# Kernel optimization log

Hardware: AMD Instinct MI355X
Metric: run time of the kernel (lower is better)

The kernel has to match this reference:

```python
import jax, jax.numpy as jnp
import numpy as np

N_CENTER, N_NEAR, N_STEPK, N_HOPS = 512, 32, 10, 2
FEAT_NAMES = ["xyz_fea", "pmt_fea", "mad_fea", "dim_fea", "nor_fea", "loc_fea", "fea"]


def pairwise_sqdist(x):
    # x: [B,N,C] -> [B,N,N]
    xx = jnp.sum(x * x, axis=-1)
    return xx[:, :, None] + xx[:, None, :] - 2.0 * jnp.einsum('bnc,bmc->bnm', x, x)


def surface_knn(x, n_near, n_stepk, n_hops=N_HOPS):
    # Iterative surface-KNN: build a step-KNN graph with n_stepk neighbors,
    # expand the neighborhood n_hops times (neighbor-of-neighbor union), then
    # pick the n_near nearest points among the reachable candidate set.
    d = pairwise_sqdist(x)                      # [B,N,N]
    B, N, _ = d.shape
    _, nbr = jax.lax.top_k(-d, n_stepk + 1)     # step neighbors (incl. self)
    b_idx = jnp.arange(B)[:, None, None]
    r_idx = jnp.arange(N)[None, :, None]
    adj = jnp.zeros((B, N, N), jnp.bool_).at[b_idx, r_idx, nbr].set(True)
    reach = adj
    adj_f = adj.astype(jnp.float32)
    for _ in range(n_hops):
        reach = (jnp.einsum('bij,bjk->bik', reach.astype(jnp.float32), adj_f) > 0) | adj
    dm = jnp.where(reach, d, jnp.inf)
    _, idx = jax.lax.top_k(-dm, n_near)         # [B,N,n_near], nearest reachable
    return idx


def fps(x, n_center):
    # Farthest point sampling in the C-dim feature space (dim=dim in source).
    B, N, _ = x.shape
    d = pairwise_sqdist(x)
    barange = jnp.arange(B)

    def step(carry, _):
        mind, prev = carry
        mind = jnp.minimum(mind, d[barange, prev])   # [B,N]
        nxt = jnp.argmax(mind, axis=-1).astype(jnp.int32)
        return (mind, nxt), nxt

    init = (jnp.full((B, N), jnp.inf, jnp.float32), jnp.zeros((B,), jnp.int32))
    _, rest = jax.lax.scan(step, init, None, length=n_center - 1)  # [S-1,B]
    idx = jnp.concatenate([jnp.zeros((1, B), jnp.int32), rest], axis=0)
    return idx.T                                   # [B,S]


def branch(center, grouped, wq, bq, wk, bk, wv, bv, w1, b1, w2, b2):
    # center: [B,S,C], grouped: [B,S,K,C]
    C = center.shape[-1]
    q = center @ wq + bq                           # [B,S,C]
    k = grouped @ wk + bk                          # [B,S,K,C]
    v = grouped @ wv + bv
    scores = jnp.einsum('bsc,bskc->bsk', q, k) / jnp.sqrt(jnp.float32(C))
    attn = jax.nn.softmax(scores, axis=-1)
    out = jnp.einsum('bsk,bskc->bsc', attn, v)     # attention pooling -> [B,S,C]
    h = jax.nn.relu(out @ w1 + b1)                 # MLP (C -> Cout -> Cout)
    return jax.nn.relu(h @ w2 + b2)


def setup_inputs() -> dict:
    key = jax.random.key(0)
    ks = jax.random.split(key, 16)
    B, N, C, CO = 8, 2048, 128, 256
    inp = {}
    for i, name in enumerate(FEAT_NAMES):
        inp[name] = jax.random.normal(ks[i], (B, N, C), jnp.float32)
    s = np.float32(1.0 / np.sqrt(C))
    so = np.float32(1.0 / np.sqrt(CO))
    inp['aw_q'] = jax.random.normal(ks[7], (7, C, C), jnp.float32) * s
    inp['ab_q'] = jnp.zeros((7, C), jnp.float32)
    inp['aw_k'] = jax.random.normal(ks[8], (7, C, C), jnp.float32) * s
    inp['ab_k'] = jnp.zeros((7, C), jnp.float32)
    inp['aw_v'] = jax.random.normal(ks[9], (7, C, C), jnp.float32) * s
    inp['ab_v'] = jnp.zeros((7, C), jnp.float32)
    inp['mw1'] = jax.random.normal(ks[10], (7, C, CO), jnp.float32) * s
    inp['mb1'] = jnp.zeros((7, CO), jnp.float32)
    inp['mw2'] = jax.random.normal(ks[11], (7, CO, CO), jnp.float32) * so
    inp['mb2'] = jnp.zeros((7, CO), jnp.float32)
    return inp


def reference(xyz_fea, pmt_fea, mad_fea, dim_fea, nor_fea, loc_fea, fea,
              aw_q, ab_q, aw_k, ab_k, aw_v, ab_v, mw1, mb1, mw2, mb2):
    B = xyz_fea.shape[0]
    feats = jnp.stack([xyz_fea, pmt_fea, mad_fea, dim_fea, nor_fea, loc_fea, fea], 0)  # [7,B,N,C]
    idx_all = surface_knn(xyz_fea, N_NEAR, N_STEPK)      # [B,N,K]
    fps_idx = fps(xyz_fea, N_CENTER)                     # [B,S]
    b2 = jnp.arange(B)[:, None]                          # [B,1]
    b3 = jnp.arange(B)[:, None, None]                    # [B,1,1]
    centers = feats[:, b2, fps_idx]                      # [7,B,S,C]
    idx = idx_all[b2, fps_idx]                           # [B,S,K]
    grouped = feats[:, b3, idx]                          # [7,B,S,K,C]
    outs = jax.vmap(branch)(centers, grouped, aw_q, ab_q, aw_k, ab_k,
                            aw_v, ab_v, mw1, mb1, mw2, mb2)  # [7,B,S,CO]
    return tuple(outs[i] for i in range(7))
```

## Files before the change

### kernel.cpp

```cpp
#include <hip/hip_runtime.h>
#include <hip/hip_bf16.h>
#include <math.h>

constexpr int BATCH = 8;
constexpr int NPTS  = 2048;
constexpr int CH    = 128;
constexpr int CHO   = 256;
constexpr int NCEN  = 512;
constexpr int NNEI  = 32;
constexpr int NTOP  = 11;
constexpr int NW    = 64;
constexpr int SMEM_BYTES = 17408;
constexpr int SMEM_MID   = 20608;

struct Ptr7 { const float* p[7]; };

__global__ __launch_bounds__(256) void xx_kernel(const float* __restrict__ x,
                                                 float* __restrict__ xx) {
    int p = blockIdx.x * 256 + threadIdx.x;
    if (p >= BATCH * NPTS) return;
    const float4* xr = (const float4*)(x + (size_t)p * CH);
    float s = 0.f;
#pragma unroll
    for (int i = 0; i < CH / 4; i++) {
        float4 v = xr[i];
        s += v.x * v.x + v.y * v.y + v.z * v.z + v.w * v.w;
    }
    xx[p] = s;
}

__global__ __launch_bounds__(256) void dmat_kernel(const float* __restrict__ x,
                                                   const float* __restrict__ xx,
                                                   float* __restrict__ D) {
    __shared__ __align__(16) char smem[SMEM_BYTES];
    int it = blockIdx.y, jt = blockIdx.x;
    if (jt < it) return;
    float (*As)[68] = (float(*)[68])smem;
    float (*Bs)[68] = (float(*)[68])(smem + 32 * 68 * 4);
    int bz = blockIdx.z;
    int i0 = it * 64, j0 = jt * 64;
    const float* X = x + (size_t)bz * NPTS * CH;
    int t = threadIdx.x, tx = t & 15, ty = t >> 4;
    int lr = t >> 3, lc = (t & 7) * 4;
    const float* ai0 = X + (size_t)(i0 + lr) * CH;
    const float* ai1 = X + (size_t)(i0 + lr + 32) * CH;
    const float* bj0 = X + (size_t)(j0 + lr) * CH;
    const float* bj1 = X + (size_t)(j0 + lr + 32) * CH;
    float acc[4][4] = {};
    for (int kc = 0; kc < CH; kc += 32) {
        float4 a0 = *(const float4*)(ai0 + kc + lc);
        float4 a1 = *(const float4*)(ai1 + kc + lc);
        float4 b0 = *(const float4*)(bj0 + kc + lc);
        float4 b1 = *(const float4*)(bj1 + kc + lc);
        __syncthreads();
        As[lc + 0][lr] = a0.x; As[lc + 1][lr] = a0.y; As[lc + 2][lr] = a0.z; As[lc + 3][lr] = a0.w;
        As[lc + 0][lr + 32] = a1.x; As[lc + 1][lr + 32] = a1.y; As[lc + 2][lr + 32] = a1.z; As[lc + 3][lr + 32] = a1.w;
        Bs[lc + 0][lr] = b0.x; Bs[lc + 1][lr] = b0.y; Bs[lc + 2][lr] = b0.z; Bs[lc + 3][lr] = b0.w;
        Bs[lc + 0][lr + 32] = b1.x; Bs[lc + 1][lr + 32] = b1.y; Bs[lc + 2][lr + 32] = b1.z; Bs[lc + 3][lr + 32] = b1.w;
        __syncthreads();
#pragma unroll
        for (int kk = 0; kk < 32; kk++) {
            float4 av = *(const float4*)&As[kk][ty * 4];
            float4 bv = *(const float4*)&Bs[kk][tx * 4];
            float a[4] = {av.x, av.y, av.z, av.w};
            float b[4] = {bv.x, bv.y, bv.z, bv.w};
#pragma unroll
            for (int i = 0; i < 4; i++)
#pragma unroll
                for (int j = 0; j < 4; j++) acc[i][j] += a[i] * b[j];
        }
    }
    const float* xxb = xx + bz * NPTS;
    float xi[4], xj[4];
#pragma unroll
    for (int i = 0; i < 4; i++) xi[i] = xxb[i0 + ty * 4 + i];
#pragma unroll
    for (int j = 0; j < 4; j++) xj[j] = xxb[j0 + tx * 4 + j];
    float ov[4][4];
#pragma unroll
    for (int i = 0; i < 4; i++)
#pragma unroll
        for (int j = 0; j < 4; j++) ov[i][j] = xi[i] + xj[j] - 2.f * acc[i][j];
#pragma unroll
    for (int i = 0; i < 4; i++) {
        float4 o = {ov[i][0], ov[i][1], ov[i][2], ov[i][3]};
        *(float4*)(D + ((size_t)bz * NPTS + i0 + ty * 4 + i) * NPTS + j0 + tx * 4) = o;
    }
    if (jt > it) {
        __syncthreads();
        float (*T)[65] = (float(*)[65])smem;
#pragma unroll
        for (int i = 0; i < 4; i++)
#pragma unroll
            for (int j = 0; j < 4; j++) T[ty * 4 + i][tx * 4 + j] = ov[i][j];
        __syncthreads();
#pragma unroll
        for (int i = 0; i < 4; i++) {
            float4 o;
            o.x = T[tx * 4 + 0][ty * 4 + i];
            o.y = T[tx * 4 + 1][ty * 4 + i];
            o.z = T[tx * 4 + 2][ty * 4 + i];
            o.w = T[tx * 4 + 3][ty * 4 + i];
            *(float4*)(D + ((size_t)bz * NPTS + j0 + ty * 4 + i) * NPTS + i0 + tx * 4) = o;
        }
    }
}

__global__ __launch_bounds__(256) void fused_front_kernel(const float* __restrict__ D,
                                                          unsigned int* __restrict__ adj,
                                                          int* __restrict__ fps_idx) {
    __shared__ __align__(16) char smem[SMEM_BYTES];
    if (blockIdx.x < BATCH) {
        int lane = threadIdx.x;
        if (lane >= 64) return;
        int b = blockIdx.x;
        float mind[32];
#pragma unroll
        for (int r = 0; r < 32; r++) mind[r] = INFINITY;
        int prev = 0;
        if (lane == 0) fps_idx[b * NCEN] = 0;
        const float* Db = D + (size_t)b * NPTS * NPTS;
        for (int s = 1; s < NCEN; s++) {
            const float4* rowp = (const float4*)(Db + (size_t)prev * NPTS);
            float4 v0 = rowp[lane + 0 * 64];
            float4 v1 = rowp[lane + 1 * 64];
            float4 v2 = rowp[lane + 2 * 64];
            float4 v3 = rowp[lane + 3 * 64];
            float4 v4 = rowp[lane + 4 * 64];
            float4 v5 = rowp[lane + 5 * 64];
            float4 v6 = rowp[lane + 6 * 64];
            float4 v7 = rowp[lane + 7 * 64];
            float bv = -INFINITY; int bj = NPTS;
            float4 vv[8] = {v0, v1, v2, v3, v4, v5, v6, v7};
#pragma unroll
            for (int k = 0; k < 8; k++) {
                int j0 = 4 * (lane + 64 * k);
                float m0 = fminf(mind[4 * k + 0], vv[k].x); mind[4 * k + 0] = m0;
                float m1 = fminf(mind[4 * k + 1], vv[k].y); mind[4 * k + 1] = m1;
                float m2 = fminf(mind[4 * k + 2], vv[k].z); mind[4 * k + 2] = m2;
                float m3 = fminf(mind[4 * k + 3], vv[k].w); mind[4 * k + 3] = m3;
                if (m0 > bv) { bv = m0; bj = j0 + 0; }
                if (m1 > bv) { bv = m1; bj = j0 + 1; }
                if (m2 > bv) { bv = m2; bj = j0 + 2; }
                if (m3 > bv) { bv = m3; bj = j0 + 3; }
            }
#pragma unroll
            for (int off = 32; off > 0; off >>= 1) {
                float ov = __shfl_xor(bv, off);
                int oj = __shfl_xor(bj, off);
                if (ov > bv || (ov == bv && oj < bj)) { bv = ov; bj = oj; }
            }
            if (lane == 0) fps_idx[b * NCEN + s] = bj;
            prev = bj;
        }
        return;
    }
    float* row = (float*)smem;
    float* rv = row + NPTS;
    int* ri = (int*)(rv + 256);
    int* picks = ri + 256;
    int rid = blockIdx.x - BATCH;
    const float* Dr = D + (size_t)rid * NPTS;
    int t = threadIdx.x;
    float4* rp = (float4*)row;
    rp[t] = ((const float4*)Dr)[t];
    rp[t + 256] = ((const float4*)Dr)[t + 256];
    __syncthreads();
    for (int it = 0; it < NTOP; it++) {
        float bv = row[t];
        int bi = t;
#pragma unroll
        for (int k = 1; k < 8; k++) {
            int j = t + (k << 8);
            float v = row[j];
            if (v < bv) { bv = v; bi = j; }
        }
        rv[t] = bv; ri[t] = bi;
        __syncthreads();
        for (int off = 128; off > 0; off >>= 1) {
            if (t < off) {
                float ovv = rv[t + off]; int oi = ri[t + off];
                if (ovv < rv[t] || (ovv == rv[t] && oi < ri[t])) { rv[t] = ovv; ri[t] = oi; }
            }
            __syncthreads();
        }
        if (t == 0) { picks[it] = ri[0]; row[ri[0]] = INFINITY; }
        __syncthreads();
    }
    if (t < NW) {
        unsigned w = 0;
#pragma unroll
        for (int p = 0; p < NTOP; p++) {
            int j = picks[p];
            if ((j >> 5) == t) w |= 1u << (j & 31);
        }
        adj[(size_t)rid * NW + t] = w;
    }
}

__global__ void make_gather(const int* __restrict__ fps_idx, int* __restrict__ gatherC) {
    int r = blockIdx.x * 256 + threadIdx.x;
    if (r >= BATCH * NCEN) return;
    int b = r >> 9, s = r & 511;
    gatherC[r] = b * NPTS + fps_idx[b * NCEN + s];
}

template <int KSIZE, bool RELU>
__device__ __forceinline__ void gemm_tile64(char* smem,
                                            const float* __restrict__ A, int lda,
                                            const int* __restrict__ gather,
                                            const float* __restrict__ W, int ldw,
                                            const float* __restrict__ bias,
                                            float* __restrict__ Out, int ldo) {
    float (*As)[68] = (float(*)[68])smem;
    float (*Ws)[68] = (float(*)[68])(smem + 32 * 68 * 4);
    int t = threadIdx.x;
    int tx = t & 15, ty = t >> 4;
    int lr = t >> 3, lc = (t & 7) * 4;
    const float* ar0 = A + (size_t)(gather ? gather[lr] : lr) * lda;
    const float* ar1 = A + (size_t)(gather ? gather[lr + 32] : lr + 32) * lda;
    float acc[4][4] = {};
    for (int kc = 0; kc < KSIZE; kc += 32) {
        float4 a0 = *(const float4*)(ar0 + kc + lc);
        float4 a1 = *(const float4*)(ar1 + kc + lc);
        float4 w0 = *(const float4*)(W + (size_t)(kc + lr) * ldw + lc);
        float4 w1 = *(const float4*)(W + (size_t)(kc + lr) * ldw + lc + 32);
        __syncthreads();
        As[lc + 0][lr] = a0.x; As[lc + 1][lr] = a0.y; As[lc + 2][lr] = a0.z; As[lc + 3][lr] = a0.w;
        As[lc + 0][lr + 32] = a1.x; As[lc + 1][lr + 32] = a1.y; As[lc + 2][lr + 32] = a1.z; As[lc + 3][lr + 32] = a1.w;
        *(float4*)&Ws[lr][lc] = w0;
        *(float4*)&Ws[lr][lc + 32] = w1;
        __syncthreads();
#pragma unroll
        for (int kk = 0; kk < 32; kk++) {
            float4 av = *(const float4*)&As[kk][ty * 4];
            float4 wv = *(const float4*)&Ws[kk][tx * 4];
            float a[4] = {av.x, av.y, av.z, av.w};
            float w[4] = {wv.x, wv.y, wv.z, wv.w};
#pragma unroll
            for (int i = 0; i < 4; i++)
#pragma unroll
                for (int j = 0; j < 4; j++) acc[i][j] += a[i] * w[j];
        }
    }
#pragma unroll
    for (int i = 0; i < 4; i++) {
        int r = ty * 4 + i;
        float4 o;
        o.x = acc[i][0] + bias[tx * 4 + 0];
        o.y = acc[i][1] + bias[tx * 4 + 1];
        o.z = acc[i][2] + bias[tx * 4 + 2];
        o.w = acc[i][3] + bias[tx * 4 + 3];
        if (RELU) {
            o.x = fmaxf(o.x, 0.f); o.y = fmaxf(o.y, 0.f);
            o.z = fmaxf(o.z, 0.f); o.w = fmaxf(o.w, 0.f);
        }
        *(float4*)(Out + (size_t)r * ldo + tx * 4) = o;
    }
}

__global__ __launch_bounds__(256) void fused_mid_kernel(const unsigned int* __restrict__ adj,
                                                        const float* __restrict__ D,
                                                        const int* __restrict__ fps_idx,
                                                        int* __restrict__ idx_sel,
                                                        Ptr7 feats,
                                                        const float* __restrict__ awq,
                                                        const float* __restrict__ abq,
                                                        const int* __restrict__ gatherC,
                                                        float* __restrict__ qtab) {
    __shared__ __align__(16) char smem[SMEM_MID];
    if (blockIdx.x >= NCEN * BATCH) {
        int id = blockIdx.x - NCEN * BATCH;
        int rt = id & 63;
        int ct = (id >> 6) & 1;
        int v = id >> 7;
        gemm_tile64<CH, false>(smem, feats.p[v], CH, gatherC + rt * 64,
                               awq + (size_t)v * CH * CH + ct * 64, CH,
                               abq + v * CH + ct * 64,
                               qtab + ((size_t)v * (BATCH * NCEN) + rt * 64) * CH + ct * 64, CH);
        return;
    }
    unsigned* adjw = (unsigned*)smem;
    unsigned* R1 = adjw + NW;
    unsigned* R2 = R1 + NW;
    int* cnt = (int*)(R2 + NW);
    int* lst = (int*)(smem + 1024);
    float* dst = (float*)(smem + 1024 + 8192);
    float* rv = (float*)(smem + 1024 + 16384);
    int* rj = (int*)(smem + 1024 + 16384 + 1024);
    int* rp = (int*)(smem + 1024 + 16384 + 2048);
    int* sel = (int*)(smem + 1024 + 16384 + 3072);
    int s = blockIdx.x & (NCEN - 1), b = blockIdx.x >> 9, t = threadIdx.x;
    int i = fps_idx[b * NCEN + s];
    const unsigned* arow = adj + ((size_t)(b * NPTS + i)) * NW;
    if (t < NW) { adjw[t] = arow[t]; R1[t] = arow[t]; }
    if (t == 0) cnt[0] = 0;
    __syncthreads();
    if (t < NW) {
        unsigned w = adjw[t];
        while (w) { int bb = __ffs(w) - 1; w &= w - 1; int p = atomicAdd(cnt, 1); lst[p] = t * 32 + bb; }
    }
    __syncthreads();
    int n1 = cnt[0];
    {
        int g = t >> 6, lane = t & 63;
        for (int p = g; p < n1; p += 4) {
            unsigned aw = adj[((size_t)(b * NPTS + lst[p])) * NW + lane];
            atomicOr(&R1[lane], aw);
        }
    }
    __syncthreads();
    if (t == 0) cnt[0] = 0;
    __syncthreads();
    if (t < NW) {
        unsigned w = R1[t];
        while (w) { int bb = __ffs(w) - 1; w &= w - 1; int p = atomicAdd(cnt, 1); lst[p] = t * 32 + bb; }
        R2[t] = adjw[t];
    }
    __syncthreads();
    int n2 = cnt[0];
    {
        int g = t >> 6, lane = t & 63;
        for (int p = g; p < n2; p += 4) {
            unsigned aw = adj[((size_t)(b * NPTS + lst[p])) * NW + lane];
            atomicOr(&R2[lane], aw);
        }
    }
    __syncthreads();
    if (t == 0) cnt[0] = 0;
    __syncthreads();
    const float* Dr = D + (size_t)(b * NPTS + i) * NPTS;
    if (t < NW) {
        unsigned w = R2[t];
        while (w) {
            int bb = __ffs(w) - 1; w &= w - 1;
            int j = t * 32 + bb;
            int p = atomicAdd(cnt, 1);
            lst[p] = j; dst[p] = Dr[j];
        }
    }
    __syncthreads();
    int L = cnt[0];
    int nsel = L < NNEI ? L : NNEI;
    for (int r = 0; r < nsel; r++) {
        float bv = INFINITY; int bj = 0x7fffffff, bp = -1;
        for (int p = t; p < L; p += 256) {
            float v = dst[p]; int j = lst[p];
            if (v < bv || (v == bv && j < bj)) { bv = v; bj = j; bp = p; }
        }
        rv[t] = bv; rj[t] = bj; rp[t] = bp;
        __syncthreads();
        for (int off = 128; off > 0; off >>= 1) {
            if (t < off) {
                if (rv[t + off] < rv[t] || (rv[t + off] == rv[t] && rj[t + off] < rj[t])) {
                    rv[t] = rv[t + off]; rj[t] = rj[t + off]; rp[t] = rp[t + off];
                }
            }
            __syncthreads();
        }
        if (t == 0) { sel[r] = rj[0]; dst[rp[0]] = INFINITY; }
        __syncthreads();
    }
    if (t == 0 && nsel < NNEI) {
        int r = nsel;
        for (int j = 0; j < NPTS && r < NNEI; j++)
            if (!((R2[j >> 5] >> (j & 31)) & 1)) sel[r++] = j;
    }
    __syncthreads();
    if (t < NNEI) idx_sel[((size_t)(b * NCEN + s)) * NNEI + t] = sel[t];
}

__global__ __launch_bounds__(256) void kvproj_kernel(Ptr7 feats, const float* __restrict__ awk,
                                                     const float* __restrict__ abk,
                                                     const float* __restrict__ awv,
                                                     const float* __restrict__ abv,
                                                     float* __restrict__ ktab,
                                                     float* __restrict__ vtab) {
    __shared__ __align__(16) char smem[SMEM_BYTES];
    int v = blockIdx.z, ct = blockIdx.y, rt = blockIdx.x;
    bool isv = ct >= 2;
    int c2 = ct & 1;
    const float* A = feats.p[v] + (size_t)rt * 64 * CH;
    const float* W = (isv ? awv : awk) + (size_t)v * CH * CH + c2 * 64;
    const float* bias = (isv ? abv : abk) + v * CH + c2 * 64;
    float* Out = (isv ? vtab : ktab) + (size_t)v * (BATCH * NPTS) * CH + (size_t)rt * 64 * CH + c2 * 64;
    gemm_tile64<CH, false>(smem, A, CH, nullptr, W, CH, bias, Out, CH);
}

__global__ __launch_bounds__(256) void mlp1_kernel(const float* __restrict__ otab,
                                                   const float* __restrict__ mw1,
                                                   const float* __restrict__ mb1,
                                                   float* __restrict__ htab) {
    __shared__ __align__(16) char smem[SMEM_BYTES];
    int v = blockIdx.z, ct = blockIdx.y, rt = blockIdx.x;
    gemm_tile64<CH, true>(smem, otab + ((size_t)v * (BATCH * NCEN) + rt * 64) * CH, CH, nullptr,
                          mw1 + (size_t)v * CH * CHO + ct * 64, CHO,
                          mb1 + v * CHO + ct * 64,
                          htab + ((size_t)v * (BATCH * NCEN) + rt * 64) * CHO + ct * 64, CHO);
}

__global__ __launch_bounds__(256) void mlp2_kernel(const float* __restrict__ htab,
                                                   const float* __restrict__ mw2,
                                                   const float* __restrict__ mb2,
                                                   float* __restrict__ out) {
    __shared__ __align__(16) char smem[SMEM_BYTES];
    int v = blockIdx.z, ct = blockIdx.y, rt = blockIdx.x;
    gemm_tile64<CHO, true>(smem, htab + ((size_t)v * (BATCH * NCEN) + rt * 64) * CHO, CHO, nullptr,
                           mw2 + (size_t)v * CHO * CHO + ct * 64, CHO,
                           mb2 + v * CHO + ct * 64,
                           out + ((size_t)v * (BATCH * NCEN) + rt * 64) * CHO + ct * 64, CHO);
}

__global__ __launch_bounds__(256) void attn_kernel(const float* __restrict__ qtab,
                                                   const float* __restrict__ ktab,
                                                   const float* __restrict__ vtab,
                                                   const int* __restrict__ idx_sel,
                                                   float* __restrict__ otab) {
    __shared__ float q_s[4][CH];
    __shared__ float attn_s[4][NNEI];
    __shared__ int jj_s[4][NNEI];
    int v = blockIdx.y;
    int t = threadIdx.x, w = t >> 6, lane = t & 63;
    int cg = blockIdx.x * 4 + w;
    int b = cg >> 9, s = cg & 511;
    const float* qr = qtab + ((size_t)v * (BATCH * NCEN) + cg) * CH;
    *(float2*)&q_s[w][lane * 2] = *(const float2*)(qr + lane * 2);
    if (lane < NNEI) jj_s[w][lane] = idx_sel[((size_t)(b * NCEN + s)) * NNEI + lane];
    __syncthreads();
    if (lane < NNEI) {
        int j = jj_s[w][lane];
        const float* kr = ktab + ((size_t)v * (BATCH * NPTS) + b * NPTS + j) * CH;
        float acc = 0.f;
#pragma unroll
        for (int c4 = 0; c4 < CH / 4; c4++) {
            float4 qv = *(const float4*)&q_s[w][c4 * 4];
            float4 kv = *(const float4*)(kr + c4 * 4);
            acc += qv.x * kv.x + qv.y * kv.y + qv.z * kv.z + qv.w * kv.w;
        }
        float sc = acc * 0.08838834764831845f;
        float m = sc;
#pragma unroll
        for (int off = 16; off > 0; off >>= 1) m = fmaxf(m, __shfl_xor(m, off, 32));
        float e = expf(sc - m);
        float sum = e;
#pragma unroll
        for (int off = 16; off > 0; off >>= 1) sum += __shfl_xor(sum, off, 32);
        attn_s[w][lane] = e / sum;
    }
    __syncthreads();
    float2 o = {0.f, 0.f};
    const float* vbase = vtab + ((size_t)v * (BATCH * NPTS) + b * NPTS) * CH;
    for (int tt = 0; tt < NNEI; tt++) {
        int j = jj_s[w][tt];
        float a = attn_s[w][tt];
        float2 vv = *(const float2*)(vbase + (size_t)j * CH + lane * 2);
        o.x += a * vv.x;
        o.y += a * vv.y;
    }
    *(float2*)(otab + ((size_t)v * (BATCH * NCEN) + cg) * CH + lane * 2) = o;
}

extern "C" void kernel_launch(void* const* d_in, const int* in_sizes, int n_in,
                              void* d_out, int out_size, void* d_ws, size_t ws_size,
                              hipStream_t stream) {
    (void)in_sizes; (void)n_in; (void)out_size;
    Ptr7 feats;
    for (int i = 0; i < 7; i++) feats.p[i] = (const float*)d_in[i];
    const float* awq = (const float*)d_in[7];
    const float* abq = (const float*)d_in[8];
    const float* awk = (const float*)d_in[9];
    const float* abk = (const float*)d_in[10];
    const float* awv = (const float*)d_in[11];
    const float* abv = (const float*)d_in[12];
    const float* mw1 = (const float*)d_in[13];
    const float* mb1 = (const float*)d_in[14];
    const float* mw2 = (const float*)d_in[15];
    const float* mb2 = (const float*)d_in[16];
    const float* xyz = feats.p[0];

    char* ws = (char*)d_ws;
    size_t SZ_D = (size_t)BATCH * NPTS * NPTS * 4;
    float* D = (float*)ws;
    float* ktab = (float*)ws;
    float* vtab = (float*)(ws + (size_t)7 * BATCH * NPTS * CH * 4);
    size_t off = SZ_D;
    float* xx = (float*)(ws + off); off += (size_t)BATCH * NPTS * 4;
    unsigned* adjb = (unsigned*)(ws + off); off += (size_t)BATCH * NPTS * NW * 4;
    int* fpsidx = (int*)(ws + off); off += (size_t)BATCH * NCEN * 4;
    int* idxsel = (int*)(ws + off); off += (size_t)BATCH * NCEN * NNEI * 4;
    int* gatherC = (int*)(ws + off); off += (size_t)BATCH * NCEN * 4;
    float* qtab = (float*)(ws + off); off += (size_t)7 * BATCH * NCEN * CH * 4;
    float* otab = (float*)(ws + off); off += (size_t)7 * BATCH * NCEN * CH * 4;
    float* htab = (float*)(ws + off); off += (size_t)7 * BATCH * NCEN * CHO * 4;
    if (ws_size < off) return;

    xx_kernel<<<dim3((BATCH * NPTS + 255) / 256), dim3(256), 0, stream>>>(xyz, xx);
    dmat_kernel<<<dim3(NPTS / 64, NPTS / 64, BATCH), dim3(256), 0, stream>>>(xyz, xx, D);
    fused_front_kernel<<<dim3(BATCH + BATCH * NPTS), dim3(256), 0, stream>>>(D, adjb, fpsidx);
    make_gather<<<dim3((BATCH * NCEN + 255) / 256), dim3(256), 0, stream>>>(fpsidx, gatherC);
    fused_mid_kernel<<<dim3(NCEN * BATCH + 2 * 7 * (BATCH * NCEN / 64)), dim3(256), 0, stream>>>(
        adjb, D, fpsidx, idxsel, feats, awq, abq, gatherC, qtab);
    kvproj_kernel<<<dim3(BATCH * NPTS / 64, 4, 7), dim3(256), 0, stream>>>(feats, awk, abk, awv, abv, ktab, vtab);
    attn_kernel<<<dim3(BATCH * NCEN / 4, 7), dim3(256), 0, stream>>>(qtab, ktab, vtab, idxsel, otab);
    mlp1_kernel<<<dim3(BATCH * NCEN / 64, 4, 7), dim3(256), 0, stream>>>(otab, mw1, mb1, htab);
    mlp2_kernel<<<dim3(BATCH * NCEN / 64, 4, 7), dim3(256), 0, stream>>>(htab, mw2, mb2, (float*)d_out);
}
```

Measured before the change: 1.170 ms.

## Use single-wavefront shuffle top-k selection and keep FPS min-distances in LDS

The per-center nearest-32 selection loop now runs on a single 64-lane wavefront. It uses xor-shuffle argmin reductions instead of a 256-thread shared-memory tree with many block barriers per round, which is meant to remove barrier and LDS traffic from the selection phase. Separately, the FPS wave keeps its running min-distance array in shared memory instead of 32 registers, presumably to cut register pressure in the fused front kernel. That second change adds an LDS read and write per element on the serial FPS critical path.

Result: faster. 1.132 ms (-3.2%).

```diff
diff --git a/kernel.cpp b/kernel.cpp
--- a/kernel.cpp
+++ b/kernel.cpp
@@ -114,35 +114,39 @@
         int lane = threadIdx.x;
         if (lane >= 64) return;
         int b = blockIdx.x;
-        float mind[32];
-#pragma unroll
-        for (int r = 0; r < 32; r++) mind[r] = INFINITY;
+        float4* mp = (float4*)smem;
+        float4 inf4 = {INFINITY, INFINITY, INFINITY, INFINITY};
+#pragma unroll
+        for (int k = 0; k < 8; k++) mp[lane + 64 * k] = inf4;
         int prev = 0;
         if (lane == 0) fps_idx[b * NCEN] = 0;
         const float* Db = D + (size_t)b * NPTS * NPTS;
         for (int s = 1; s < NCEN; s++) {
             const float4* rowp = (const float4*)(Db + (size_t)prev * NPTS);
-            float4 v0 = rowp[lane + 0 * 64];
-            float4 v1 = rowp[lane + 1 * 64];
-            float4 v2 = rowp[lane + 2 * 64];
-            float4 v3 = rowp[lane + 3 * 64];
-            float4 v4 = rowp[lane + 4 * 64];
-            float4 v5 = rowp[lane + 5 * 64];
-            float4 v6 = rowp[lane + 6 * 64];
-            float4 v7 = rowp[lane + 7 * 64];
+            float4 g0 = rowp[lane + 0 * 64];
+            float4 g1 = rowp[lane + 1 * 64];
+            float4 g2 = rowp[lane + 2 * 64];
+            float4 g3 = rowp[lane + 3 * 64];
+            float4 g4 = rowp[lane + 4 * 64];
+            float4 g5 = rowp[lane + 5 * 64];
+            float4 g6 = rowp[lane + 6 * 64];
+            float4 g7 = rowp[lane + 7 * 64];
+            float4 gg[8] = {g0, g1, g2, g3, g4, g5, g6, g7};
             float bv = -INFINITY; int bj = NPTS;
-            float4 vv[8] = {v0, v1, v2, v3, v4, v5, v6, v7};
 #pragma unroll
             for (int k = 0; k < 8; k++) {
-                int j0 = 4 * (lane + 64 * k);
-                float m0 = fminf(mind[4 * k + 0], vv[k].x); mind[4 * k + 0] = m0;
-                float m1 = fminf(mind[4 * k + 1], vv[k].y); mind[4 * k + 1] = m1;
-                float m2 = fminf(mind[4 * k + 2], vv[k].z); mind[4 * k + 2] = m2;
-                float m3 = fminf(mind[4 * k + 3], vv[k].w); mind[4 * k + 3] = m3;
-                if (m0 > bv) { bv = m0; bj = j0 + 0; }
-                if (m1 > bv) { bv = m1; bj = j0 + 1; }
-                if (m2 > bv) { bv = m2; bj = j0 + 2; }
-                if (m3 > bv) { bv = m3; bj = j0 + 3; }
+                int li = lane + 64 * k;
+                float4 m = mp[li];
+                m.x = fminf(m.x, gg[k].x);
+                m.y = fminf(m.y, gg[k].y);
+                m.z = fminf(m.z, gg[k].z);
+                m.w = fminf(m.w, gg[k].w);
+                mp[li] = m;
+                int j0 = 4 * li;
+                if (m.x > bv) { bv = m.x; bj = j0 + 0; }
+                if (m.y > bv) { bv = m.y; bj = j0 + 1; }
+                if (m.z > bv) { bv = m.z; bj = j0 + 2; }
+                if (m.w > bv) { bv = m.w; bj = j0 + 3; }
             }
 #pragma unroll
             for (int off = 32; off > 0; off >>= 1) {
@@ -286,10 +290,7 @@
     int* cnt = (int*)(R2 + NW);
     int* lst = (int*)(smem + 1024);
     float* dst = (float*)(smem + 1024 + 8192);
-    float* rv = (float*)(smem + 1024 + 16384);
-    int* rj = (int*)(smem + 1024 + 16384 + 1024);
-    int* rp = (int*)(smem + 1024 + 16384 + 2048);
-    int* sel = (int*)(smem + 1024 + 16384 + 3072);
+    int* sel = (int*)(smem + 1024 + 16384);
     int s = blockIdx.x & (NCEN - 1), b = blockIdx.x >> 9, t = threadIdx.x;
     int i = fps_idx[b * NCEN + s];
     const unsigned* arow = adj + ((size_t)(b * NPTS + i)) * NW;
@@ -340,34 +341,31 @@
         }
     }
     __syncthreads();
+    if (t >= 64) return;
     int L = cnt[0];
     int nsel = L < NNEI ? L : NNEI;
+    int lane = t;
     for (int r = 0; r < nsel; r++) {
         float bv = INFINITY; int bj = 0x7fffffff, bp = -1;
-        for (int p = t; p < L; p += 256) {
+        for (int p = lane; p < L; p += 64) {
             float v = dst[p]; int j = lst[p];
             if (v < bv || (v == bv && j < bj)) { bv = v; bj = j; bp = p; }
         }
-        rv[t] = bv; rj[t] = bj; rp[t] = bp;
-        __syncthreads();
-        for (int off = 128; off > 0; off >>= 1) {
-            if (t < off) {
-                if (rv[t + off] < rv[t] || (rv[t + off] == rv[t] && rj[t + off] < rj[t])) {
-                    rv[t] = rv[t + off]; rj[t] = rj[t + off]; rp[t] = rp[t + off];
-                }
-            }
-            __syncthreads();
-        }
-        if (t == 0) { sel[r] = rj[0]; dst[rp[0]] = INFINITY; }
-        __syncthreads();
-    }
-    if (t == 0 && nsel < NNEI) {
+#pragma unroll
+        for (int off = 32; off > 0; off >>= 1) {
+            float ov = __shfl_xor(bv, off);
+            int oj = __shfl_xor(bj, off);
+            int op = __shfl_xor(bp, off);
+            if (ov < bv || (ov == bv && oj < bj)) { bv = ov; bj = oj; bp = op; }
+        }
+        if (lane == 0) { sel[r] = bj; dst[bp] = INFINITY; }
+    }
+    if (lane == 0 && nsel < NNEI) {
         int r = nsel;
         for (int j = 0; j < NPTS && r < NNEI; j++)
             if (!((R2[j >> 5] >> (j & 31)) & 1)) sel[r++] = j;
     }
-    __syncthreads();
-    if (t < NNEI) idx_sel[((size_t)(b * NCEN + s)) * NNEI + t] = sel[t];
+    if (lane < NNEI) idx_sel[((size_t)(b * NCEN + s)) * NNEI + lane] = sel[lane];
 }
 
 __global__ __launch_bounds__(256) void kvproj_kernel(Ptr7 feats, const float* __restrict__ awk,
```
